# Kernel optimization log

Measured on AMD Instinct MI355X. Metric: run time of the kernel, lower is better.

## Reference

```python
import jax, jax.numpy as jnp
import numpy as np

B, S, D, F = 8, 4096, 1024, 3072
EPS = 1e-6

def rmsnorm(x, w):
    rms = jax.lax.rsqrt(jnp.mean(x * x, axis=-1, keepdims=True) + EPS)
    return x * rms * w

def linear_scan(x, a):
    # h_t = a_t * h_{t-1} + x_t, causal over axis 1 (h_0 prior state = 0)
    def combine(c1, c2):
        a1, h1 = c1
        a2, h2 = c2
        return a1 * a2, a2 * h1 + h2
    return jax.lax.associative_scan(combine, (a, x), axis=1)[1]

def setup_inputs() -> dict:
    key = jax.random.key(0)
    ks = jax.random.split(key, 10)
    s_d = 1.0 / np.sqrt(D)
    s_f = 1.0 / np.sqrt(F)
    return {
        "x": jax.random.normal(ks[0], (B, S, D), jnp.float32),
        "w_rms_mix": jnp.ones((D,), jnp.float32),
        "w_rms_ffn": jnp.ones((D,), jnp.float32),
        "Wg": jax.random.normal(ks[1], (D, D), jnp.float32) * s_d,
        "bg": jnp.zeros((D,), jnp.float32),
        "Wv": jax.random.normal(ks[2], (D, D), jnp.float32) * s_d,
        "bv": jnp.zeros((D,), jnp.float32),
        "Wd": jax.random.normal(ks[3], (D, D), jnp.float32) * s_d,
        "bd": jnp.ones((D,), jnp.float32),  # decay_bias_init = 1.0
        "W_gate": jax.random.normal(ks[4], (D, F), jnp.float32) * s_d,
        "W_up": jax.random.normal(ks[5], (D, F), jnp.float32) * s_d,
        "W_out": jax.random.normal(ks[6], (F, D), jnp.float32) * s_f,
    }

def reference(x, w_rms_mix, w_rms_ffn, Wg, bg, Wv, bv, Wd, bd, W_gate, W_up, W_out):
    # --- MinGRU mixer branch ---
    xn = rmsnorm(x, w_rms_mix)
    g = xn @ Wg + bg
    v = xn @ Wv + bv
    d = xn @ Wd + bd
    x_scan = jax.nn.sigmoid(g) * jnp.tanh(v)
    a = 0.001 + 0.998 * jax.nn.sigmoid(d)
    x = x + linear_scan(x_scan, a)
    # --- SwiGLU FFN branch ---
    yn = rmsnorm(x, w_rms_ffn)
    ffn = (jax.nn.silu(yn @ W_gate) * (yn @ W_up)) @ W_out
    return x + ffn
```

## Files before the change

### kernel.cpp

```cpp
#include <hip/hip_runtime.h>

#define BB 8
#define SS 4096
#define DDIM 1024
#define FDIM 3072
#define CHUNK 128
#define NCH (SS/CHUNK)

typedef __attribute__((ext_vector_type(8))) __bf16 bf16x8;
typedef __attribute__((ext_vector_type(4))) float f32x4;

__device__ __forceinline__ unsigned short f2bf(float f) {
  unsigned int u = __builtin_bit_cast(unsigned int, f);
  u += 0x7FFFu + ((u >> 16) & 1u);
  return (unsigned short)(u >> 16);
}
__device__ __forceinline__ float sigmoid_(float x) { return 1.0f / (1.0f + __expf(-x)); }
__device__ __forceinline__ float tanh_(float x) {
  float xc = fminf(fmaxf(x, -15.0f), 15.0f);
  float e = __expf(2.0f * xc);
  return (e - 1.0f) / (e + 1.0f);
}

__global__ __launch_bounds__(256)
void pack_w(const float* __restrict__ src, unsigned short* __restrict__ dst,
            int Csrc, int Kd, int mode, int rowoff)
{
  __shared__ float tile[64][65];
  const int k0 = blockIdx.y << 6;
  const int c0 = blockIdx.x << 6;
  const int t  = threadIdx.x;
  const int tc = t & 63;
  const int tr = t >> 6;
#pragma unroll
  for (int j = 0; j < 16; j++) {
    int r = (j << 2) + tr;
    tile[r][tc] = src[(size_t)(k0 + r) * Csrc + c0 + tc];
  }
  __syncthreads();
#pragma unroll
  for (int j = 0; j < 16; j++) {
    int c  = (j << 2) + tr;
    int gc = c0 + c;
    int np;
    if (mode == 0)      np = gc + rowoff;
    else if (mode == 1) np = ((gc >> 5) << 6) + (gc & 31);
    else if (mode == 2) np = ((gc >> 5) << 6) + 32 + (gc & 31);
    else                np = ((gc >> 4) << 6) + ((mode - 3) << 4) + (gc & 15);
    dst[(size_t)np * Kd + k0 + tc] = f2bf(tile[tc][c]);
    if (mode == 5) dst[(size_t)(np + 16) * Kd + k0 + tc] = 0;
  }
}

__global__ void pack_bias(const float* __restrict__ bg, const float* __restrict__ bv,
                          const float* __restrict__ bd, float* __restrict__ bias)
{
  int i = blockIdx.x * 256 + threadIdx.x;
  if (i < DDIM) { bias[i] = bg[i]; bias[i + DDIM] = bv[i]; bias[i + 2 * DDIM] = bd[i]; }
}

__global__ __launch_bounds__(256)
void rmsnorm_kernel(const float* __restrict__ x, const float* __restrict__ w,
                    unsigned short* __restrict__ out)
{
  const int row = blockIdx.x;
  const int t = threadIdx.x;
  const float4 v = reinterpret_cast<const float4*>(x + (size_t)row * DDIM)[t];
  float ss = v.x * v.x + v.y * v.y + v.z * v.z + v.w * v.w;
#pragma unroll
  for (int o = 32; o > 0; o >>= 1) ss += __shfl_down(ss, o);
  __shared__ float wsum[4];
  if ((t & 63) == 0) wsum[t >> 6] = ss;
  __syncthreads();
  float tot = wsum[0] + wsum[1] + wsum[2] + wsum[3];
  const float rms = rsqrtf(tot * (1.0f / DDIM) + 1e-6f);
  const float4 wv = reinterpret_cast<const float4*>(w)[t];
  ushort4 o4;
  o4.x = f2bf(v.x * rms * wv.x);
  o4.y = f2bf(v.y * rms * wv.y);
  o4.z = f2bf(v.z * rms * wv.z);
  o4.w = f2bf(v.w * rms * wv.w);
  reinterpret_cast<ushort4*>(out + (size_t)row * DDIM)[t] = o4;
}


template<int MH, int NH>
__device__ __forceinline__ void mfma_quad(f32x4 (&acc)[8][4], const bf16x8 (&af)[4][2],
                                          const bf16x8 (&bfr)[2][2][2])
{
#pragma unroll
  for (int mf = 0; mf < 4; mf++)
#pragma unroll
    for (int nf = 0; nf < 2; nf++)
#pragma unroll
      for (int kk = 0; kk < 2; kk++)
        acc[MH * 4 + mf][NH * 2 + nf] = __builtin_amdgcn_mfma_f32_16x16x32_bf16(
            af[mf][kk], bfr[NH][nf][kk], acc[MH * 4 + mf][NH * 2 + nf], 0, 0, 0);
}

#define PH_PRE()  do { __builtin_amdgcn_s_barrier(); \
  asm volatile("s_waitcnt lgkmcnt(0)" ::: "memory"); \
  __builtin_amdgcn_sched_barrier(0); \
  __builtin_amdgcn_s_setprio(1); } while (0)
#define PH_POST() do { __builtin_amdgcn_s_setprio(0); \
  __builtin_amdgcn_sched_barrier(0); \
  __builtin_amdgcn_s_barrier(); \
  __builtin_amdgcn_sched_barrier(0); } while (0)

template<int EPI>
__global__ __launch_bounds__(512, 2)
void gemm256(const unsigned short* __restrict__ A,
             const unsigned short* __restrict__ Bt,
             int Np, int K,
             const float* __restrict__ bias,
             const float* __restrict__ resid,
             float* __restrict__ outf,
             unsigned short* __restrict__ outh)
{
  __shared__ __align__(16) unsigned short ldsA[2][256 * 64];
  __shared__ __align__(16) unsigned short ldsB[2][256 * 64];
  const int tid = threadIdx.x, wid = tid >> 6, lane = tid & 63;

  const int gx = gridDim.x;
  const int lin = blockIdx.y * gx + blockIdx.x;
  const int cpx = (gx * gridDim.y) >> 3;
  const int swz = (lin & 7) * cpx + (lin >> 3);
  const int bx = swz % gx, by = swz / gx;
  const int m0 = by << 8, n0 = bx << 8;
  const int wr = wid >> 2, wc = wid & 3;

  f32x4 acc[8][4];
  const f32x4 zero = {0.f, 0.f, 0.f, 0.f};
#pragma unroll
  for (int a = 0; a < 8; a++)
#pragma unroll
    for (int j = 0; j < 4; j++) acc[a][j] = zero;

  const int swzk = (((tid & 7) ^ ((tid >> 3) & 7)) << 3);
  auto stA = [&](int p, int u, int t) {
#pragma unroll
    for (int r = 0; r < 2; r++) {
      const int lrow0 = (r << 7) + (u << 6);
      const int grow = m0 + lrow0 + (tid >> 3);
      const unsigned short* src = A + (size_t)grow * K + (t << 6) + swzk;
      unsigned short* dst = &ldsA[p][lrow0 << 6] + (wid << 9);
      __builtin_amdgcn_global_load_lds(
          (const __attribute__((address_space(1))) void*)src,
          (__attribute__((address_space(3))) void*)dst, 16, 0, 0);
    }
  };
  auto stB = [&](int p, int u, int t) {
#pragma unroll
    for (int r = 0; r < 2; r++) {
      const int j = (r << 6) + (tid >> 3);
      const int lrow0 = (u << 7) + (r << 6);
      const int gcol = n0 + ((j >> 5) << 6) + (u << 5) + (j & 31);
      const unsigned short* src = Bt + (size_t)gcol * K + (t << 6) + swzk;
      unsigned short* dst = &ldsB[p][lrow0 << 6] + (wid << 9);
      __builtin_amdgcn_global_load_lds(
          (const __attribute__((address_space(1))) void*)src,
          (__attribute__((address_space(3))) void*)dst, 16, 0, 0);
    }
  };

  bf16x8 af[4][2];
  bf16x8 bfr[2][2][2];
  auto rdA = [&](const unsigned short* base, int mh) {
#pragma unroll
    for (int mf = 0; mf < 4; mf++) {
      const int row = (wr << 7) + (mh << 6) + (mf << 4) + (lane & 15);
#pragma unroll
      for (int kk = 0; kk < 2; kk++) {
        const int keb = (((kk << 6) + ((lane >> 4) << 4)) ^ ((lane & 7) << 4));
        af[mf][kk] = *reinterpret_cast<const bf16x8*>(
            reinterpret_cast<const char*>(base) + (row << 7) + keb);
      }
    }
  };
  auto rdB = [&](const unsigned short* base, bf16x8 (&dst)[2][2], int nh) {
#pragma unroll
    for (int nf = 0; nf < 2; nf++) {
      const int row = (nh << 7) + (wc << 5) + (nf << 4) + (lane & 15);
#pragma unroll
      for (int kk = 0; kk < 2; kk++) {
        const int keb = (((kk << 6) + ((lane >> 4) << 4)) ^ ((lane & 7) << 4));
        dst[nf][kk] = *reinterpret_cast<const bf16x8*>(
            reinterpret_cast<const char*>(base) + (row << 7) + keb);
      }
    }
  };

  const int NITER = (K >> 6) >> 1;

  stA(0, 0, 0); stA(0, 1, 0); stB(0, 0, 0); stB(0, 1, 0);
  stA(1, 0, 1); stB(1, 0, 1);
  asm volatile("s_waitcnt vmcnt(4)" ::: "memory");
  __builtin_amdgcn_s_barrier();
  __builtin_amdgcn_sched_barrier(0);

  for (int i = 0; i < NITER; i++) {
    const int t2 = i << 1;
    const bool more = (i + 1 < NITER);
    rdA(ldsA[0], 0);
    rdB(ldsB[0], bfr[0], 0);
    stA(1, 1, t2 + 1);
    PH_PRE();
    mfma_quad<0, 0>(acc, af, bfr);
    PH_POST();
    rdB(ldsB[0], bfr[1], 1);
    stB(1, 1, t2 + 1);
    PH_PRE();
    mfma_quad<0, 1>(acc, af, bfr);
    PH_POST();
    rdA(ldsA[0], 1);
    if (more) stA(0, 0, t2 + 2);
    PH_PRE();
    mfma_quad<1, 0>(acc, af, bfr);
    PH_POST();
    if (more) stB(0, 0, t2 + 2);
    PH_PRE();
    mfma_quad<1, 1>(acc, af, bfr);
    __builtin_amdgcn_s_setprio(0);
    __builtin_amdgcn_sched_barrier(0);
    if (more) { asm volatile("s_waitcnt vmcnt(4)" ::: "memory"); }
    else      { asm volatile("s_waitcnt vmcnt(0)" ::: "memory"); }
    __builtin_amdgcn_s_barrier();
    __builtin_amdgcn_sched_barrier(0);
    rdA(ldsA[1], 0);
    rdB(ldsB[1], bfr[0], 0);
    if (more) stA(0, 1, t2 + 2);
    PH_PRE();
    mfma_quad<0, 0>(acc, af, bfr);
    PH_POST();
    rdB(ldsB[1], bfr[1], 1);
    if (more) stB(0, 1, t2 + 2);
    PH_PRE();
    mfma_quad<0, 1>(acc, af, bfr);
    PH_POST();
    rdA(ldsA[1], 1);
    if (more) stA(1, 0, t2 + 3);
    PH_PRE();
    mfma_quad<1, 0>(acc, af, bfr);
    PH_POST();
    if (more) stB(1, 0, t2 + 3);
    PH_PRE();
    mfma_quad<1, 1>(acc, af, bfr);
    __builtin_amdgcn_s_setprio(0);
    __builtin_amdgcn_sched_barrier(0);
    if (more) { asm volatile("s_waitcnt vmcnt(4)" ::: "memory"); }
    __builtin_amdgcn_s_barrier();
    __builtin_amdgcn_sched_barrier(0);
  }

  const int lcol = lane & 15;
  const int rgrp = (lane >> 4) << 2;
  if (EPI == 0) {
    const int ch = (n0 >> 2) + (wc << 4) + lcol;
    const float bgv = bias[ch], bvv = bias[ch + DDIM], bdv = bias[ch + 2 * DDIM];
#pragma unroll
    for (int a = 0; a < 8; a++)
#pragma unroll
      for (int rg = 0; rg < 4; rg++) {
        const int row = m0 + (wr << 7) + (a << 4) + rgrp + rg;
        const float g  = acc[a][0][rg] + bgv;
        const float v  = acc[a][1][rg] + bvv;
        const float dd = acc[a][2][rg] + bdv;
        const float aa = 0.001f + 0.998f * sigmoid_(dd);
        const float xs = sigmoid_(g) * tanh_(v);
        float* o = outf + (size_t)row * (2 * DDIM);
        o[ch] = aa;
        o[ch + DDIM] = xs;
      }
  } else if (EPI == 1) {
    const int tN = Np >> 1;
#pragma unroll
    for (int a = 0; a < 8; a++)
#pragma unroll
      for (int j = 0; j < 2; j++) {
        const int tcol = (n0 >> 1) + (wc << 5) + (j << 4) + lcol;
#pragma unroll
        for (int rg = 0; rg < 4; rg++) {
          const int row = m0 + (wr << 7) + (a << 4) + rgrp + rg;
          const float g = acc[a][j][rg];
          const float u = acc[a][j + 2][rg];
          const float s = g / (1.0f + __expf(-g));
          outh[(size_t)row * tN + tcol] = f2bf(s * u);
        }
      }
  } else {
#pragma unroll
    for (int a = 0; a < 8; a++)
#pragma unroll
      for (int j = 0; j < 4; j++) {
        const int col = n0 + (wc << 6) + (j << 4) + lcol;
#pragma unroll
        for (int rg = 0; rg < 4; rg++) {
          const int row = m0 + (wr << 7) + (a << 4) + rgrp + rg;
          outf[(size_t)row * Np + col] = acc[a][j][rg] + resid[(size_t)row * Np + col];
        }
      }
  }
}

__global__ __launch_bounds__(256)
void scan_phase1(const float* __restrict__ ax, float* __restrict__ Ac, float* __restrict__ Hc)
{
  const int d = blockIdx.x * 256 + threadIdx.x;
  const int ch = blockIdx.y;
  const int b = blockIdx.z;
  size_t base = ((size_t)b * SS + (size_t)ch * CHUNK) * (2 * DDIM) + d;
  float Aprod = 1.0f, H = 0.0f;
  for (int s = 0; s < CHUNK; s++) {
    const float a  = ax[base];
    const float xs = ax[base + DDIM];
    H = a * H + xs;
    Aprod *= a;
    base += 2 * DDIM;
  }
  const int idx = (b * NCH + ch) * DDIM + d;
  Ac[idx] = Aprod;
  Hc[idx] = H;
}

__global__ void scan_phase2(const float* __restrict__ Ac, const float* __restrict__ Hc,
                            float* __restrict__ Hpre)
{
  const int idx = blockIdx.x * 256 + threadIdx.x;
  const int b = idx >> 10, d = idx & (DDIM - 1);
  float h = 0.0f;
  for (int c = 0; c < NCH; c++) {
    const int i = (b * NCH + c) * DDIM + d;
    Hpre[i] = h;
    h = Ac[i] * h + Hc[i];
  }
}

__global__ __launch_bounds__(256)
void scan_phase3(const float* __restrict__ ax, const float* __restrict__ x,
                 const float* __restrict__ Hpre, float* __restrict__ xres)
{
  const int d = blockIdx.x * 256 + threadIdx.x;
  const int ch = blockIdx.y;
  const int b = blockIdx.z;
  float H = Hpre[(b * NCH + ch) * DDIM + d];
  const size_t mbase = (size_t)b * SS + (size_t)ch * CHUNK;
  size_t base  = mbase * (2 * DDIM) + d;
  size_t xbase = mbase * DDIM + d;
  for (int s = 0; s < CHUNK; s++) {
    const float a  = ax[base];
    const float xs = ax[base + DDIM];
    H = a * H + xs;
    xres[xbase] = x[xbase] + H;
    base += 2 * DDIM;
    xbase += DDIM;
  }
}

extern "C" void kernel_launch(void* const* d_in, const int* in_sizes, int n_in,
                              void* d_out, int out_size, void* d_ws, size_t ws_size,
                              hipStream_t stream)
{
  const float* x         = (const float*)d_in[0];
  const float* w_rms_mix = (const float*)d_in[1];
  const float* w_rms_ffn = (const float*)d_in[2];
  const float* Wg  = (const float*)d_in[3];
  const float* bg  = (const float*)d_in[4];
  const float* Wv  = (const float*)d_in[5];
  const float* bv  = (const float*)d_in[6];
  const float* Wd  = (const float*)d_in[7];
  const float* bd  = (const float*)d_in[8];
  const float* Wga = (const float*)d_in[9];
  const float* Wup = (const float*)d_in[10];
  const float* Wo  = (const float*)d_in[11];
  float* out = (float*)d_out;

  char* p = (char*)d_ws;
  auto carve = [&](size_t bytes) -> char* {
    char* r = p; p += (bytes + 255) & ~(size_t)255; return r;
  };
  unsigned short* Wgvd4 = (unsigned short*)carve((size_t)4 * DDIM * DDIM * 2);
  unsigned short* WguT  = (unsigned short*)carve((size_t)2 * FDIM * DDIM * 2);
  unsigned short* WoutT = (unsigned short*)carve((size_t)DDIM * FDIM * 2);
  float* bias = (float*)carve(3 * DDIM * 4);
  const size_t fixed_used = (size_t)(p - (char*)d_ws);

  const size_t xn_b  = (size_t)SS * DDIM * 2;
  const size_t ax_b  = (size_t)SS * 2 * DDIM * 4;
  const size_t ach_b = (size_t)NCH * DDIM * 4;
  const size_t per_batch = xn_b + ax_b + 3 * ach_b + 2048;
  long long avail = (long long)ws_size - (long long)fixed_used;
  int nb = (avail > 0) ? (int)(avail / (long long)per_batch) : 1;
  if (nb < 1) nb = 1;
  if (nb > BB) nb = BB;

  unsigned short* xn = (unsigned short*)carve((size_t)nb * xn_b);
  float* ax   = (float*)carve((size_t)nb * ax_b);
  unsigned short* tact = (unsigned short*)ax;
  float* Ac   = (float*)carve((size_t)nb * ach_b);
  float* Hc   = (float*)carve((size_t)nb * ach_b);
  float* Hpre = (float*)carve((size_t)nb * ach_b);

  pack_w<<<dim3(16, 16), 256, 0, stream>>>(Wg,  Wgvd4, DDIM, DDIM, 3, 0);
  pack_w<<<dim3(16, 16), 256, 0, stream>>>(Wv,  Wgvd4, DDIM, DDIM, 4, 0);
  pack_w<<<dim3(16, 16), 256, 0, stream>>>(Wd,  Wgvd4, DDIM, DDIM, 5, 0);
  pack_w<<<dim3(48, 16), 256, 0, stream>>>(Wga, WguT,  FDIM, DDIM, 1, 0);
  pack_w<<<dim3(48, 16), 256, 0, stream>>>(Wup, WguT,  FDIM, DDIM, 2, 0);
  pack_w<<<dim3(16, 48), 256, 0, stream>>>(Wo,  WoutT, DDIM, FDIM, 0, 0);
  pack_bias<<<4, 256, 0, stream>>>(bg, bv, bd, bias);

  for (int b0 = 0; b0 < BB; b0 += nb) {
    const int n  = (BB - b0 < nb) ? (BB - b0) : nb;
    const int Mg = n * SS;
    const float* xg   = x   + (size_t)b0 * SS * DDIM;
    float*       outg = out + (size_t)b0 * SS * DDIM;

    rmsnorm_kernel<<<Mg, 256, 0, stream>>>(xg, w_rms_mix, xn);

    gemm256<0><<<dim3(4 * DDIM / 256, Mg / 256), 512, 0, stream>>>(
        xn, Wgvd4, 4 * DDIM, DDIM, bias, nullptr, ax, nullptr);

    scan_phase1<<<dim3(DDIM / 256, NCH, n), 256, 0, stream>>>(ax, Ac, Hc);
    scan_phase2<<<(n * DDIM) / 256, 256, 0, stream>>>(Ac, Hc, Hpre);
    scan_phase3<<<dim3(DDIM / 256, NCH, n), 256, 0, stream>>>(ax, xg, Hpre, outg);

    rmsnorm_kernel<<<Mg, 256, 0, stream>>>(outg, w_rms_ffn, xn);

    gemm256<1><<<dim3(2 * FDIM / 256, Mg / 256), 512, 0, stream>>>(
        xn, WguT, 2 * FDIM, DDIM, nullptr, nullptr, nullptr, tact);

    gemm256<2><<<dim3(DDIM / 256, Mg / 256), 512, 0, stream>>>(
        tact, WoutT, DDIM, FDIM, nullptr, outg, outg, nullptr);
  }
}
```

Before: 1.140 ms.

## Reschedule GEMM main loop with double-buffered fragments and inline-asm LDS reads

Rewrites the 256x256 GEMM inner loop so LDS fragment reads for the next quad are issued before the current MFMA block. It uses two B-fragment register sets, inline ds_read_b128 with precomputed addresses and immediate offsets, and partial lgkmcnt/vmcnt waits instead of full drains. The global-to-LDS prefetch order is changed to keep more loads in flight. For the fused gate/value/decay projection (EPI 0) it skips the MFMAs for the unused fourth column fragment. This raises register pressure, and the hand-tuned wait counts and barriers risk races if they are miscounted.

Result: faster. 1.054 ms (-7.5%).

```diff
diff --git a/kernel.cpp b/kernel.cpp
--- a/kernel.cpp
+++ b/kernel.cpp
@@ -84,28 +84,38 @@
 }
 
 
-template<int MH, int NH>
+#define SB0 __builtin_amdgcn_sched_barrier(0)
+#define BAR __builtin_amdgcn_s_barrier()
+#define PRIO1 __builtin_amdgcn_s_setprio(1)
+#define PRIO0 __builtin_amdgcn_s_setprio(0)
+#define WAITL4 do { asm volatile("s_waitcnt lgkmcnt(4)" ::: "memory"); SB0; } while (0)
+#define WAITL0 do { asm volatile("s_waitcnt lgkmcnt(0)" ::: "memory"); SB0; } while (0)
+#define WAITV6 do { asm volatile("s_waitcnt vmcnt(6)" ::: "memory"); } while (0)
+#define WAITV0 do { asm volatile("s_waitcnt vmcnt(0)" ::: "memory"); } while (0)
+
+#define DSR(D, A, O) asm volatile("ds_read_b128 %0, %1 offset:" O : "=v"(D) : "v"(A))
+#define RD_AF(O0, O1, O2, O3) do { \
+  DSR(af[0][0], aA0, O0); DSR(af[0][1], aA1, O0); \
+  DSR(af[1][0], aA0, O1); DSR(af[1][1], aA1, O1); \
+  DSR(af[2][0], aA0, O2); DSR(af[2][1], aA1, O2); \
+  DSR(af[3][0], aA0, O3); DSR(af[3][1], aA1, O3); } while (0)
+#define RD_BF(B, O0, O1) do { \
+  DSR(B[0][0], bB0, O0); DSR(B[0][1], bB1, O0); \
+  DSR(B[1][0], bB0, O1); DSR(B[1][1], bB1, O1); } while (0)
+
+template<int MH, int NH, bool SKIP1>
 __device__ __forceinline__ void mfma_quad(f32x4 (&acc)[8][4], const bf16x8 (&af)[4][2],
-                                          const bf16x8 (&bfr)[2][2][2])
+                                          const bf16x8 (&bf)[2][2])
 {
 #pragma unroll
   for (int mf = 0; mf < 4; mf++)
 #pragma unroll
-    for (int nf = 0; nf < 2; nf++)
+    for (int nf = 0; nf < (SKIP1 ? 1 : 2); nf++)
 #pragma unroll
       for (int kk = 0; kk < 2; kk++)
         acc[MH * 4 + mf][NH * 2 + nf] = __builtin_amdgcn_mfma_f32_16x16x32_bf16(
-            af[mf][kk], bfr[NH][nf][kk], acc[MH * 4 + mf][NH * 2 + nf], 0, 0, 0);
-}
-
-#define PH_PRE()  do { __builtin_amdgcn_s_barrier(); \
-  asm volatile("s_waitcnt lgkmcnt(0)" ::: "memory"); \
-  __builtin_amdgcn_sched_barrier(0); \
-  __builtin_amdgcn_s_setprio(1); } while (0)
-#define PH_POST() do { __builtin_amdgcn_s_setprio(0); \
-  __builtin_amdgcn_sched_barrier(0); \
-  __builtin_amdgcn_s_barrier(); \
-  __builtin_amdgcn_sched_barrier(0); } while (0)
+            af[mf][kk], bf[nf][kk], acc[MH * 4 + mf][NH * 2 + nf], 0, 0, 0);
+}
 
 template<int EPI>
 __global__ __launch_bounds__(512, 2)
@@ -120,6 +130,7 @@
   __shared__ __align__(16) unsigned short ldsA[2][256 * 64];
   __shared__ __align__(16) unsigned short ldsB[2][256 * 64];
   const int tid = threadIdx.x, wid = tid >> 6, lane = tid & 63;
+  constexpr bool SK = (EPI == 0);
 
   const int gx = gridDim.x;
   const int lin = blockIdx.y * gx + blockIdx.x;
@@ -163,94 +174,74 @@
     }
   };
 
+  const unsigned laneR = (unsigned)((lane & 15) << 7);
+  const unsigned sw    = (unsigned)((lane & 7) << 4);
+  const unsigned k0b   = (unsigned)((lane >> 4) << 4);
+  const unsigned baseA = (unsigned)(uintptr_t)&ldsA[0][0] + ((unsigned)wr << 14);
+  const unsigned baseB = (unsigned)(uintptr_t)&ldsB[0][0] + ((unsigned)wc << 12);
+  const unsigned aA0 = baseA + laneR + (k0b ^ sw);
+  const unsigned aA1 = baseA + laneR + ((64u + k0b) ^ sw);
+  const unsigned bB0 = baseB + laneR + (k0b ^ sw);
+  const unsigned bB1 = baseB + laneR + ((64u + k0b) ^ sw);
+
   bf16x8 af[4][2];
-  bf16x8 bfr[2][2][2];
-  auto rdA = [&](const unsigned short* base, int mh) {
-#pragma unroll
-    for (int mf = 0; mf < 4; mf++) {
-      const int row = (wr << 7) + (mh << 6) + (mf << 4) + (lane & 15);
-#pragma unroll
-      for (int kk = 0; kk < 2; kk++) {
-        const int keb = (((kk << 6) + ((lane >> 4) << 4)) ^ ((lane & 7) << 4));
-        af[mf][kk] = *reinterpret_cast<const bf16x8*>(
-            reinterpret_cast<const char*>(base) + (row << 7) + keb);
-      }
-    }
-  };
-  auto rdB = [&](const unsigned short* base, bf16x8 (&dst)[2][2], int nh) {
-#pragma unroll
-    for (int nf = 0; nf < 2; nf++) {
-      const int row = (nh << 7) + (wc << 5) + (nf << 4) + (lane & 15);
-#pragma unroll
-      for (int kk = 0; kk < 2; kk++) {
-        const int keb = (((kk << 6) + ((lane >> 4) << 4)) ^ ((lane & 7) << 4));
-        dst[nf][kk] = *reinterpret_cast<const bf16x8*>(
-            reinterpret_cast<const char*>(base) + (row << 7) + keb);
-      }
-    }
-  };
+  bf16x8 bf0[2][2];
+  bf16x8 bf1[2][2];
 
   const int NITER = (K >> 6) >> 1;
 
-  stA(0, 0, 0); stA(0, 1, 0); stB(0, 0, 0); stB(0, 1, 0);
-  stA(1, 0, 1); stB(1, 0, 1);
-  asm volatile("s_waitcnt vmcnt(4)" ::: "memory");
-  __builtin_amdgcn_s_barrier();
-  __builtin_amdgcn_sched_barrier(0);
+  stB(0, 0, 0); stA(0, 0, 0); stB(0, 1, 0); stA(0, 1, 0);
+  stB(1, 0, 1); stA(1, 0, 1); stB(1, 1, 1); stA(1, 1, 1);
+  asm volatile("s_waitcnt vmcnt(8)" ::: "memory");
+  BAR; SB0;
+  RD_BF(bf0, "0", "2048");
+  RD_AF("0", "2048", "4096", "6144");
 
   for (int i = 0; i < NITER; i++) {
     const int t2 = i << 1;
     const bool more = (i + 1 < NITER);
-    rdA(ldsA[0], 0);
-    rdB(ldsB[0], bfr[0], 0);
-    stA(1, 1, t2 + 1);
-    PH_PRE();
-    mfma_quad<0, 0>(acc, af, bfr);
-    PH_POST();
-    rdB(ldsB[0], bfr[1], 1);
-    stB(1, 1, t2 + 1);
-    PH_PRE();
-    mfma_quad<0, 1>(acc, af, bfr);
-    PH_POST();
-    rdA(ldsA[0], 1);
+    RD_BF(bf1, "16384", "18432");
+    WAITL4;
+    PRIO1; mfma_quad<0, 0, false>(acc, af, bf0); PRIO0; SB0;
+    if (more) stB(0, 0, t2 + 2);
+    BAR;
+    WAITL0;
+    PRIO1; mfma_quad<0, 1, SK>(acc, af, bf1); PRIO0; SB0;
+    RD_AF("8192", "10240", "12288", "14336");
     if (more) stA(0, 0, t2 + 2);
-    PH_PRE();
-    mfma_quad<1, 0>(acc, af, bfr);
-    PH_POST();
-    if (more) stB(0, 0, t2 + 2);
-    PH_PRE();
-    mfma_quad<1, 1>(acc, af, bfr);
-    __builtin_amdgcn_s_setprio(0);
-    __builtin_amdgcn_sched_barrier(0);
-    if (more) { asm volatile("s_waitcnt vmcnt(4)" ::: "memory"); }
-    else      { asm volatile("s_waitcnt vmcnt(0)" ::: "memory"); }
-    __builtin_amdgcn_s_barrier();
-    __builtin_amdgcn_sched_barrier(0);
-    rdA(ldsA[1], 0);
-    rdB(ldsB[1], bfr[0], 0);
+    BAR;
+    WAITL0;
+    PRIO1; mfma_quad<1, 0, false>(acc, af, bf0); PRIO0; SB0;
+    if (more) stB(0, 1, t2 + 2);
+    if (more) WAITV6; else WAITV0;
+    BAR;
+    RD_BF(bf0, "32768", "34816");
+    PRIO1; mfma_quad<1, 1, SK>(acc, af, bf1); PRIO0; SB0;
+    RD_AF("32768", "34816", "36864", "38912");
     if (more) stA(0, 1, t2 + 2);
-    PH_PRE();
-    mfma_quad<0, 0>(acc, af, bfr);
-    PH_POST();
-    rdB(ldsB[1], bfr[1], 1);
-    if (more) stB(0, 1, t2 + 2);
-    PH_PRE();
-    mfma_quad<0, 1>(acc, af, bfr);
-    PH_POST();
-    rdA(ldsA[1], 1);
+    BAR;
+    RD_BF(bf1, "49152", "51200");
+    WAITL4;
+    PRIO1; mfma_quad<0, 0, false>(acc, af, bf0); PRIO0; SB0;
+    if (more) stB(1, 0, t2 + 3);
+    BAR;
+    WAITL0;
+    PRIO1; mfma_quad<0, 1, SK>(acc, af, bf1); PRIO0; SB0;
+    RD_AF("40960", "43008", "45056", "47104");
     if (more) stA(1, 0, t2 + 3);
-    PH_PRE();
-    mfma_quad<1, 0>(acc, af, bfr);
-    PH_POST();
-    if (more) stB(1, 0, t2 + 3);
-    PH_PRE();
-    mfma_quad<1, 1>(acc, af, bfr);
-    __builtin_amdgcn_s_setprio(0);
-    __builtin_amdgcn_sched_barrier(0);
-    if (more) { asm volatile("s_waitcnt vmcnt(4)" ::: "memory"); }
-    __builtin_amdgcn_s_barrier();
-    __builtin_amdgcn_sched_barrier(0);
-  }
+    BAR;
+    WAITL0;
+    PRIO1; mfma_quad<1, 0, false>(acc, af, bf0); PRIO0; SB0;
+    if (more) stB(1, 1, t2 + 3);
+    if (more) WAITV6;
+    BAR;
+    RD_BF(bf0, "0", "2048");
+    PRIO1; mfma_quad<1, 1, SK>(acc, af, bf1); PRIO0; SB0;
+    RD_AF("0", "2048", "4096", "6144");
+    if (more) stA(1, 1, t2 + 3);
+    BAR;
+  }
+  asm volatile("s_waitcnt lgkmcnt(0)" ::: "memory"); SB0;
 
   const int lcol = lane & 15;
   const int rgrp = (lane >> 4) << 2;
```
